# Kernel tuning notes

Hardware: AMD Instinct MI355X
Metric: run time of the kernel (lower is better)

## Reference

```python
import jax, jax.numpy as jnp
import numpy as np

N_NODES = 20000
N_EDGES = 200000
F = 132            # features_dim
DEGREES = (1, 2, 3)
REPEATS = jnp.array([3, 5, 7])   # 2l+1
EV_DIM = 15
H_INV, D_INV = 4, 33   # num_heads, inv_head_dim
H_EV, D_EV = 3, 44     # len(degrees), ev_head_dim
NRB = 32


def so3_invariants(x, y):
    # per-degree inner product over the (2l+1) components -> [E, len(degrees)]
    p = x * y
    return jnp.stack([p[:, 0:3].sum(-1), p[:, 3:8].sum(-1), p[:, 8:15].sum(-1)], axis=-1)


def filter_net(rbf, evi, Wr1, br1, Wr2, br2, We1, be1, We2, be2):
    # mlp_rbf: Linear(nrb,F)->SiLU->Linear(F,F); mlp_ev: Linear(3,F//4)->SiLU->Linear(F//4,F)
    r = jax.nn.silu(rbf @ Wr1 + br1) @ Wr2 + br2
    e = jax.nn.silu(evi @ We1 + be1) @ We2 + be2
    return r + e


def setup_inputs() -> dict:
    key = jax.random.key(0)
    ks = jax.random.split(key, 32)
    s = 0.05
    inp = {
        'inv_features': jax.random.normal(ks[0], (N_NODES, F), jnp.float32),
        'ev_features': jax.random.normal(ks[1], (N_NODES, EV_DIM), jnp.float32),
        'rbf': jax.random.uniform(ks[2], (N_EDGES, NRB), jnp.float32),
        'senders': jax.random.randint(ks[3], (N_EDGES,), 0, N_NODES, jnp.int32),
        'receivers': jax.random.randint(ks[4], (N_EDGES,), 0, N_NODES, jnp.int32),
        'sh_vectors': jax.random.normal(ks[5], (N_EDGES, EV_DIM), jnp.float32),
        'cutoffs': jax.random.uniform(ks[6], (N_EDGES, 1), jnp.float32),
        # attention weights
        'W_q_inv': jax.random.normal(ks[7], (H_INV, D_INV, D_INV), jnp.float32) * s,
        'W_k_inv': jax.random.normal(ks[8], (H_INV, D_INV, D_INV), jnp.float32) * s,
        'W_v_inv': jax.random.normal(ks[9], (H_INV, D_INV, D_INV), jnp.float32) * s,
        'W_q_ev': jax.random.normal(ks[10], (H_EV, D_EV, D_EV), jnp.float32) * s,
        'W_k_ev': jax.random.normal(ks[11], (H_EV, D_EV, D_EV), jnp.float32) * s,
    }
    # two FilterNets (inv and ev), stored as [in,out] matrices
    for tag, base in (('fi', 12), ('fe', 20)):
        inp[f'{tag}_rbf_W1'] = jax.random.normal(ks[base + 0], (NRB, F), jnp.float32) * s
        inp[f'{tag}_rbf_b1'] = jnp.zeros((F,), jnp.float32)
        inp[f'{tag}_rbf_W2'] = jax.random.normal(ks[base + 1], (F, F), jnp.float32) * s
        inp[f'{tag}_rbf_b2'] = jnp.zeros((F,), jnp.float32)
        inp[f'{tag}_ev_W1'] = jax.random.normal(ks[base + 2], (len(DEGREES), F // 4), jnp.float32) * s
        inp[f'{tag}_ev_b1'] = jnp.zeros((F // 4,), jnp.float32)
        inp[f'{tag}_ev_W2'] = jax.random.normal(ks[base + 3], (F // 4, F), jnp.float32) * s
        inp[f'{tag}_ev_b2'] = jnp.zeros((F,), jnp.float32)
    # interaction block linear: (F+len(degrees)) -> (F+len(degrees))
    inp['W_int'] = jax.random.normal(ks[28], (F + len(DEGREES), F + len(DEGREES)), jnp.float32) * s
    inp['b_int'] = jnp.zeros((F + len(DEGREES),), jnp.float32)
    return inp


def _forward(inv_features, ev_features, rbf, sh_vectors, cutoffs,
             W_q_inv, W_k_inv, W_v_inv, W_q_ev, W_k_ev,
             fi, fe, W_int, b_int, senders, receivers):
    E = rbf.shape[0]
    N = inv_features.shape[0]
    # ---- EuclideanAttentionBlock ----
    ev_diff = ev_features[senders] - ev_features[receivers]          # [E, 15]
    evi = so3_invariants(ev_diff, ev_diff)                            # [E, 3]
    fw_inv = filter_net(rbf, evi, *fi).reshape(E, H_INV, D_INV)
    fw_ev = filter_net(rbf, evi, *fe).reshape(E, H_EV, D_EV)
    x_inv = inv_features.reshape(N, H_INV, D_INV)
    x_ev = inv_features.reshape(N, H_EV, D_EV)
    q_inv = jnp.einsum('Hij,NHi->NHj', W_q_inv, x_inv)[receivers]
    k_inv = jnp.einsum('Hij,NHi->NHj', W_k_inv, x_inv)[senders]
    v_inv = jnp.einsum('Hij,NHi->NHj', W_v_inv, x_inv)[senders]
    q_ev = jnp.einsum('Hij,NHi->NHj', W_q_ev, x_ev)[receivers]
    k_ev = jnp.einsum('Hij,NHi->NHj', W_k_ev, x_ev)[senders]
    alpha_inv = (q_inv * k_inv * fw_inv).sum(-1, keepdims=True) / np.sqrt(D_INV)  # [E,H,1]
    scaled_inv = cutoffs[:, None] * alpha_inv * v_inv                 # [E,H,D]
    d_inv = jax.ops.segment_sum(scaled_inv, receivers, num_segments=N).reshape(N, F)
    alpha_ev = (q_ev * k_ev * fw_ev).sum(-1) / np.sqrt(D_EV)          # [E,3]
    alpha_ev = jnp.repeat(alpha_ev, REPEATS, axis=-1, total_repeat_length=EV_DIM)
    d_ev = jax.ops.segment_sum(cutoffs * alpha_ev * sh_vectors, receivers, num_segments=N)
    att_inv = inv_features + d_inv
    att_ev = ev_features + d_ev
    # ---- InteractionBlock ----
    evi2 = so3_invariants(att_ev, att_ev)                             # [N,3]
    t = jnp.concatenate([att_inv, evi2], axis=-1) @ W_int + b_int
    d_inv2, b_ev = t[:, :F], t[:, F:]
    d_ev2 = jnp.repeat(b_ev, REPEATS, axis=-1, total_repeat_length=EV_DIM) * att_ev
    return att_inv + d_inv2, att_ev + d_ev2


def reference(inv_features, ev_features, rbf, senders, receivers, sh_vectors, cutoffs,
              W_q_inv, W_k_inv, W_v_inv, W_q_ev, W_k_ev,
              fi_rbf_W1, fi_rbf_b1, fi_rbf_W2, fi_rbf_b2, fi_ev_W1, fi_ev_b1, fi_ev_W2, fi_ev_b2,
              fe_rbf_W1, fe_rbf_b1, fe_rbf_W2, fe_rbf_b2, fe_ev_W1, fe_ev_b1, fe_ev_W2, fe_ev_b2,
              W_int, b_int):
    fi = (fi_rbf_W1, fi_rbf_b1, fi_rbf_W2, fi_rbf_b2, fi_ev_W1, fi_ev_b1, fi_ev_W2, fi_ev_b2)
    fe = (fe_rbf_W1, fe_rbf_b1, fe_rbf_W2, fe_rbf_b2, fe_ev_W1, fe_ev_b1, fe_ev_W2, fe_ev_b2)
    return _forward(inv_features, ev_features, rbf, sh_vectors, cutoffs,
                    W_q_inv, W_k_inv, W_v_inv, W_q_ev, W_k_ev,
                    fi, fe, W_int, b_int, senders, receivers)
```

## Files before the change

kernel.cpp:

```cpp
#include <hip/hip_runtime.h>


#define NN 20000
#define NE 200000
#define FD 132
#define RB 32
#define EVD 15
#define TE 64
#define KPAD 200
#define KG 192
#define NP 144
#define PNT 28
#define FNT 28

typedef __attribute__((ext_vector_type(8))) short bf16x8;
typedef __attribute__((ext_vector_type(4))) float f32x4;

__device__ __forceinline__ float silu_f(float x) {
    return x / (1.0f + __expf(-x));
}
__device__ __forceinline__ unsigned short f2bf(float x) {
    union { float f; unsigned u; } v; v.f = x;
    unsigned r = v.u + 0x7FFF + ((v.u >> 16) & 1);
    return (unsigned short)(r >> 16);
}

__global__ __launch_bounds__(256) void k_prep(
    const float* __restrict__ Wq, const float* __restrict__ Wk, const float* __restrict__ Wv,
    const float* __restrict__ fiW1, const float* __restrict__ fiW2, const float* __restrict__ fiWe2,
    const float* __restrict__ feW1, const float* __restrict__ feW2, const float* __restrict__ feWe2,
    unsigned short* __restrict__ W1Tfi, unsigned short* __restrict__ W1Tfe,
    unsigned short* __restrict__ W2Tfi, unsigned short* __restrict__ W2Tfe,
    float* __restrict__ WqP, float* __restrict__ WkP, float* __restrict__ WvP)
{
    const int gid = blockIdx.x * 256 + threadIdx.x;
    const int gs  = gridDim.x * 256;
    for (int idx = gid; idx < NP * RB; idx += gs) {
        int n = idx / RB, k = idx - n * RB;
        W1Tfi[idx] = f2bf((n < FD) ? fiW1[k * FD + n] : 0.0f);
        W1Tfe[idx] = f2bf((n < FD) ? feW1[k * FD + n] : 0.0f);
    }
    for (int idx = gid; idx < NP * KG; idx += gs) {
        int n = idx / KG, k = idx - n * KG;
        float vi = 0.0f, ve = 0.0f;
        if (n < FD) {
            if (k < FD)       { vi = fiW2[k * FD + n];          ve = feW2[k * FD + n]; }
            else if (k < 165) { vi = fiWe2[(k - FD) * FD + n];  ve = feWe2[(k - FD) * FD + n]; }
        }
        W2Tfi[idx] = f2bf(vi);
        W2Tfe[idx] = f2bf(ve);
    }
    for (int idx = gid; idx < 4 * 33 * 36; idx += gs) {
        int H = idx / (33 * 36), rem = idx - H * (33 * 36);
        int i = rem / 36, jp = rem - i * 36;
        float q = 0.f, k = 0.f, v = 0.f;
        if (jp < 33) {
            q = Wq[H * 1089 + i * 33 + jp];
            k = Wk[H * 1089 + i * 33 + jp];
            v = Wv[H * 1089 + i * 33 + jp];
        }
        WqP[idx] = q; WkP[idx] = k; WvP[idx] = v;
    }
}

__device__ __forceinline__ void proj_inv_pass(
    const float* __restrict__ wb, const float (*__restrict__ xT)[PNT],
    float* __restrict__ outp, int t, int n0)
{
    const int q = t % 36, g = t / 36;
    if (g >= 7) return;
    const int H = q / 9, jb = (q - H * 9) * 4, nb = g * 4;
    const int fb = H * 33;
    float acc[4][4] = {};
    for (int i = 0; i < 33; ++i) {
        const float4 w = *(const float4*)&wb[(fb + i) * 36 + jb];
        const float4 x = *(const float4*)&xT[fb + i][nb];
        const float xs[4] = {x.x, x.y, x.z, x.w};
        const float ws[4] = {w.x, w.y, w.z, w.w};
        #pragma unroll
        for (int r = 0; r < 4; ++r)
            #pragma unroll
            for (int c = 0; c < 4; ++c)
                acc[r][c] = fmaf(ws[c], xs[r], acc[r][c]);
    }
    #pragma unroll
    for (int c = 0; c < 4; ++c) {
        int jj = jb + c;
        if (jj >= 33) break;
        int j = H * 33 + jj;
        #pragma unroll
        for (int r = 0; r < 4; ++r) {
            int n = n0 + nb + r;
            if (n < NN) outp[n * FD + j] = acc[r][c];
        }
    }
}

__device__ __forceinline__ void proj_ev_pass(
    const float* __restrict__ wb, const float (*__restrict__ xT)[PNT],
    float* __restrict__ outp, int t, int n0)
{
    const int q = t % 33, g = t / 33;
    if (g >= 7) return;
    const int H = q / 11, jb = (q - H * 11) * 4, nb = g * 4;
    const int fb = H * 44;
    float acc[4][4] = {};
    for (int i = 0; i < 44; ++i) {
        const float4 w = *(const float4*)&wb[(fb + i) * 44 + jb];
        const float4 x = *(const float4*)&xT[fb + i][nb];
        const float xs[4] = {x.x, x.y, x.z, x.w};
        const float ws[4] = {w.x, w.y, w.z, w.w};
        #pragma unroll
        for (int r = 0; r < 4; ++r)
            #pragma unroll
            for (int c = 0; c < 4; ++c)
                acc[r][c] = fmaf(ws[c], xs[r], acc[r][c]);
    }
    #pragma unroll
    for (int c = 0; c < 4; ++c) {
        int j = fb + jb + c;
        #pragma unroll
        for (int r = 0; r < 4; ++r) {
            int n = n0 + nb + r;
            if (n < NN) outp[n * FD + j] = acc[r][c];
        }
    }
}

__global__ __launch_bounds__(256) void k_proj(
    const float* __restrict__ xin,
    const float* __restrict__ WqP, const float* __restrict__ WkP, const float* __restrict__ WvP,
    const float* __restrict__ Wqe, const float* __restrict__ Wke,
    float* __restrict__ qinv, float* __restrict__ kinv, float* __restrict__ vinv,
    float* __restrict__ qev, float* __restrict__ kev)
{
    __shared__ __align__(16) float xT[FD][PNT];
    __shared__ __align__(16) float wb[5808];
    const int t = threadIdx.x;
    const int n0 = blockIdx.x * PNT;

    for (int idx = t; idx < PNT * FD; idx += 256) {
        int nl = idx / FD, j = idx - nl * FD;
        int n = n0 + nl;
        xT[j][nl] = (n < NN) ? xin[n * FD + j] : 0.0f;
    }
    for (int idx = t; idx < 4752; idx += 256) wb[idx] = WqP[idx];
    __syncthreads();
    proj_inv_pass(wb, xT, qinv, t, n0);
    __syncthreads();
    for (int idx = t; idx < 4752; idx += 256) wb[idx] = WkP[idx];
    __syncthreads();
    proj_inv_pass(wb, xT, kinv, t, n0);
    __syncthreads();
    for (int idx = t; idx < 4752; idx += 256) wb[idx] = WvP[idx];
    __syncthreads();
    proj_inv_pass(wb, xT, vinv, t, n0);
    __syncthreads();
    for (int idx = t; idx < 5808; idx += 256) wb[idx] = Wqe[idx];
    __syncthreads();
    proj_ev_pass(wb, xT, qev, t, n0);
    __syncthreads();
    for (int idx = t; idx < 5808; idx += 256) wb[idx] = Wke[idx];
    __syncthreads();
    proj_ev_pass(wb, xT, kev, t, n0);
}

__global__ __launch_bounds__(256) void k_evi(
    const float* __restrict__ ev, const int* __restrict__ snd,
    const int* __restrict__ rcv, float* __restrict__ evi)
{
    int e = blockIdx.x * 256 + threadIdx.x;
    if (e >= NE) return;
    int s = snd[e], r = rcv[e];
    const float* ps = &ev[s * EVD];
    const float* pr = &ev[r * EVD];
    float s0 = 0.f, s1 = 0.f, s2 = 0.f;
    #pragma unroll
    for (int m = 0; m < 3; ++m)  { float d = ps[m] - pr[m]; s0 = fmaf(d, d, s0); }
    #pragma unroll
    for (int m = 3; m < 8; ++m)  { float d = ps[m] - pr[m]; s1 = fmaf(d, d, s1); }
    #pragma unroll
    for (int m = 8; m < 15; ++m) { float d = ps[m] - pr[m]; s2 = fmaf(d, d, s2); }
    evi[e * 3 + 0] = s0; evi[e * 3 + 1] = s1; evi[e * 3 + 2] = s2;
}

template<int PATH>
__global__ __launch_bounds__(256, 4) void k_edge(
    const float* __restrict__ rbf, const float* __restrict__ evi,
    const int* __restrict__ snd, const int* __restrict__ rcv,
    const float* __restrict__ cut, const float* __restrict__ sh,
    const unsigned short* __restrict__ W1T,
    const float* __restrict__ b1,
    const unsigned short* __restrict__ W2T,
    const float* __restrict__ b2,
    const float* __restrict__ We1, const float* __restrict__ be1,
    const float* __restrict__ be2,
    const float* __restrict__ qt, const float* __restrict__ kt,
    const float* __restrict__ vt, float* __restrict__ dout)
{
    __shared__ __align__(16) char lds_buf[TE * FD * 4];
    __shared__ float evl[TE * 3];
    __shared__ int   sl[TE];
    __shared__ int   rl[TE];
    __shared__ float cl[TE];
    __shared__ float al[TE * 4];

    typedef unsigned short (*HTp)[KPAD];
    HTp HT   = (HTp)lds_buf;
    float* FW = (float*)lds_buf;

    const int t    = threadIdx.x;
    const int wv   = t >> 6;
    const int ln   = t & 63;
    const int lrow = ln & 15;
    const int kseg = ln >> 4;
    const int e0   = blockIdx.x * TE;

    if (t < TE) {
        sl[t] = snd[e0 + t];
        rl[t] = rcv[e0 + t];
        cl[t] = cut[e0 + t];
    }
    for (int idx = t; idx < TE * 3; idx += 256) evl[idx] = evi[e0 * 3 + idx];
    __syncthreads();

    {
        const int erow = e0 + 16 * wv + lrow;
        const float4 ra = *(const float4*)&rbf[erow * RB + kseg * 8];
        const float4 rb = *(const float4*)&rbf[erow * RB + kseg * 8 + 4];
        bf16x8 afrag;
        afrag[0] = (short)f2bf(ra.x); afrag[1] = (short)f2bf(ra.y);
        afrag[2] = (short)f2bf(ra.z); afrag[3] = (short)f2bf(ra.w);
        afrag[4] = (short)f2bf(rb.x); afrag[5] = (short)f2bf(rb.y);
        afrag[6] = (short)f2bf(rb.z); afrag[7] = (short)f2bf(rb.w);
        #pragma unroll
        for (int nt = 0; nt < 9; ++nt) {
            const int ncol = nt * 16 + lrow;
            bf16x8 bfrag = *(const bf16x8*)&W1T[ncol * RB + kseg * 8];
            f32x4 acc = {0.f, 0.f, 0.f, 0.f};
            acc = __builtin_amdgcn_mfma_f32_16x16x32_bf16(afrag, bfrag, acc, 0, 0, 0);
            if (ncol < FD) {
                const float bias = b1[ncol];
                #pragma unroll
                for (int r = 0; r < 4; ++r)
                    HT[16 * wv + kseg * 4 + r][ncol] = f2bf(silu_f(acc[r] + bias));
            }
        }
    }
    for (int idx = t; idx < TE * 33; idx += 256) {
        int e = idx / 33, ii = idx - e * 33;
        float a = be1[ii];
        a = fmaf(evl[e * 3 + 0], We1[ii], a);
        a = fmaf(evl[e * 3 + 1], We1[33 + ii], a);
        a = fmaf(evl[e * 3 + 2], We1[66 + ii], a);
        HT[e][FD + ii] = f2bf(silu_f(a));
    }
    for (int idx = t; idx < TE * (KPAD - 165); idx += 256) {
        int e = idx / (KPAD - 165), kk = idx - e * (KPAD - 165);
        HT[e][165 + kk] = 0;
    }
    __syncthreads();

    f32x4 acc[9];
    #pragma unroll
    for (int nt = 0; nt < 9; ++nt) acc[nt] = (f32x4){0.f, 0.f, 0.f, 0.f};
    {
        const unsigned short* hrow = &HT[16 * wv + lrow][0];
        #pragma unroll
        for (int kt = 0; kt < 6; ++kt) {
            bf16x8 afrag = *(const bf16x8*)&hrow[kt * 32 + kseg * 8];
            #pragma unroll
            for (int nt = 0; nt < 9; ++nt) {
                bf16x8 bfrag = *(const bf16x8*)&W2T[(nt * 16 + lrow) * KG + kt * 32 + kseg * 8];
                acc[nt] = __builtin_amdgcn_mfma_f32_16x16x32_bf16(afrag, bfrag, acc[nt], 0, 0, 0);
            }
        }
    }
    __syncthreads();

    #pragma unroll
    for (int nt = 0; nt < 9; ++nt) {
        const int ncol = nt * 16 + lrow;
        if (ncol < FD) {
            const float bias = b2[ncol] + be2[ncol];
            #pragma unroll
            for (int r = 0; r < 4; ++r)
                FW[(16 * wv + kseg * 4 + r) * FD + ncol] = acc[nt][r] + bias;
        }
    }
    __syncthreads();

    for (int idx = t; idx < TE * FD; idx += 256) {
        int e = idx / FD, j = idx - e * FD;
        FW[idx] *= qt[rl[e] * FD + j] * kt[sl[e] * FD + j];
    }
    __syncthreads();

    if (PATH == 0) {
        {
            int e = t >> 2, H = t & 3;
            const float* fp = &FW[e * FD + H * 33];
            float a = 0.0f;
            #pragma unroll
            for (int j = 0; j < 33; ++j) a += fp[j];
            al[t] = a * cl[e] * 0.17407765595569785f;
        }
    } else {
        if (t < TE * 3) {
            int e = t / 3, H = t - e * 3;
            const float* fp = &FW[e * FD + H * 44];
            float a = 0.0f;
            #pragma unroll
            for (int j = 0; j < 44; ++j) a += fp[j];
            al[e * 4 + H] = a * cl[e] * 0.15075567228888181f;
        }
    }
    __syncthreads();

    if (PATH == 0) {
        for (int idx = t; idx < TE * FD; idx += 256) {
            int e = idx / FD, j = idx - e * FD;
            float v = al[e * 4 + j / 33] * vt[sl[e] * FD + j];
            atomicAdd(&dout[rl[e] * FD + j], v);
        }
    } else {
        for (int idx = t; idx < TE * EVD; idx += 256) {
            int e = idx / EVD, m = idx - e * EVD;
            int hd = (m < 3) ? 0 : ((m < 8) ? 1 : 2);
            float v = al[e * 4 + hd] * sh[(e0 + e) * EVD + m];
            atomicAdd(&dout[rl[e] * EVD + m], v);
        }
    }
}

__global__ __launch_bounds__(256) void k_final(
    const float* __restrict__ xin, const float* __restrict__ evf,
    const float* __restrict__ dinv, const float* __restrict__ dev,
    const float* __restrict__ Wint, const float* __restrict__ bint,
    float* __restrict__ out)
{
    __shared__ __align__(16) float catT[136][FNT];
    __shared__ __align__(16) float wb[45 * 136];
    __shared__ float aev[FNT][16];
    __shared__ float tacc[FNT][4];
    const int t = threadIdx.x;
    const int n0 = blockIdx.x * FNT;

    for (int idx = t; idx < FNT * FD; idx += 256) {
        int nl = idx / FD, j = idx - nl * FD;
        int n = n0 + nl;
        catT[j][nl] = (n < NN) ? xin[n * FD + j] + dinv[n * FD + j] : 0.0f;
    }
    for (int idx = t; idx < FNT * EVD; idx += 256) {
        int nl = idx / EVD, m = idx - nl * EVD;
        int n = n0 + nl;
        aev[nl][m] = (n < NN) ? evf[n * EVD + m] + dev[n * EVD + m] : 0.0f;
    }
    if (t < FNT) catT[135][t] = 0.0f;
    __syncthreads();
    if (t < FNT * 3) {
        int nl = t / 3, k = t - nl * 3;
        int lo = (k == 0) ? 0 : ((k == 1) ? 3 : 8);
        int hi = (k == 0) ? 3 : ((k == 1) ? 8 : 15);
        float s = 0.f;
        for (int m = lo; m < hi; ++m) { float v = aev[nl][m]; s = fmaf(v, v, s); }
        catT[FD + k][nl] = s;
    }

    const int q = t % 34, g = t / 34;
    const int jb = q * 4, nb = g * 4;
    const bool act = (g < 7);
    float acc[4][4] = {};
    for (int ch = 0; ch < 3; ++ch) {
        __syncthreads();
        const int rbase = ch * 45;
        for (int idx = t; idx < 45 * 136; idx += 256) {
            int r = idx / 136, j = idx - r * 136;
            wb[idx] = (j < 135) ? Wint[(rbase + r) * 135 + j] : 0.0f;
        }
        __syncthreads();
        if (act) {
            for (int c = 0; c < 45; ++c) {
                const float4 w = *(const float4*)&wb[c * 136 + jb];
                const float4 x = *(const float4*)&catT[rbase + c][nb];
                const float xs[4] = {x.x, x.y, x.z, x.w};
                const float ws[4] = {w.x, w.y, w.z, w.w};
                #pragma unroll
                for (int r = 0; r < 4; ++r)
                    #pragma unroll
                    for (int cc = 0; cc < 4; ++cc)
                        acc[r][cc] = fmaf(ws[cc], xs[r], acc[r][cc]);
            }
        }
    }
    if (act) {
        #pragma unroll
        for (int c = 0; c < 4; ++c) {
            int j = jb + c;
            if (j >= 135) break;
            float bj = bint[j];
            #pragma unroll
            for (int r = 0; r < 4; ++r) {
                int n = n0 + nb + r;
                if (n >= NN) continue;
                float a = acc[r][c] + bj;
                if (j < FD) out[n * FD + j] = catT[j][nb + r] + a;
                else        tacc[nb + r][j - FD] = a;
            }
        }
    }
    __syncthreads();
    for (int idx = t; idx < FNT * EVD; idx += 256) {
        int nl = idx / EVD, m = idx - nl * EVD;
        int n = n0 + nl;
        if (n >= NN) continue;
        int hd = (m < 3) ? 0 : ((m < 8) ? 1 : 2);
        out[NN * FD + n * EVD + m] = aev[nl][m] * (1.0f + tacc[nl][hd]);
    }
}

extern "C" void kernel_launch(void* const* d_in, const int* in_sizes, int n_in,
                              void* d_out, int out_size, void* d_ws, size_t ws_size,
                              hipStream_t stream)
{
    (void)in_sizes; (void)n_in; (void)out_size; (void)ws_size;
    const float* xin  = (const float*)d_in[0];
    const float* evf  = (const float*)d_in[1];
    const float* rbf  = (const float*)d_in[2];
    const int*   snd  = (const int*)d_in[3];
    const int*   rcv  = (const int*)d_in[4];
    const float* sh   = (const float*)d_in[5];
    const float* cut  = (const float*)d_in[6];
    const float* Wint = (const float*)d_in[28];
    const float* bint = (const float*)d_in[29];

    float* ws   = (float*)d_ws;
    float* qinv = ws;
    float* kinv = qinv + NN * FD;
    float* vinv = kinv + NN * FD;
    float* qev  = vinv + NN * FD;
    float* kev  = qev  + NN * FD;
    float* evi  = kev  + NN * FD;
    float* dinv = evi  + NE * 3;
    float* dev  = dinv + NN * FD;
    float* wtail = dev + NN * EVD;

    unsigned short* W2Tfi = (unsigned short*)wtail;
    unsigned short* W2Tfe = W2Tfi + NP * KG;
    unsigned short* W1Tfi = W2Tfe + NP * KG;
    unsigned short* W1Tfe = W1Tfi + NP * RB;
    float* WqP = (float*)(W1Tfe + NP * RB);
    float* WkP = WqP + 4 * 33 * 36;
    float* WvP = WkP + 4 * 33 * 36;

    hipMemsetAsync(dinv, 0, (size_t)(NN * FD + NN * EVD) * sizeof(float), stream);

    k_prep<<<64, 256, 0, stream>>>(
        (const float*)d_in[7], (const float*)d_in[8], (const float*)d_in[9],
        (const float*)d_in[12], (const float*)d_in[14], (const float*)d_in[18],
        (const float*)d_in[20], (const float*)d_in[22], (const float*)d_in[26],
        W1Tfi, W1Tfe, W2Tfi, W2Tfe, WqP, WkP, WvP);

    k_proj<<<(NN + PNT - 1) / PNT, 256, 0, stream>>>(
        xin, WqP, WkP, WvP,
        (const float*)d_in[10], (const float*)d_in[11],
        qinv, kinv, vinv, qev, kev);
    k_evi<<<(NE + 255) / 256, 256, 0, stream>>>(evf, snd, rcv, evi);

    const int nt = NE / TE;
    k_edge<0><<<nt, 256, 0, stream>>>(rbf, evi, snd, rcv, cut, sh,
        W1Tfi, (const float*)d_in[13], W2Tfi, (const float*)d_in[15],
        (const float*)d_in[16], (const float*)d_in[17], (const float*)d_in[19],
        qinv, kinv, vinv, dinv);
    k_edge<1><<<nt, 256, 0, stream>>>(rbf, evi, snd, rcv, cut, sh,
        W1Tfe, (const float*)d_in[21], W2Tfe, (const float*)d_in[23],
        (const float*)d_in[24], (const float*)d_in[25], (const float*)d_in[27],
        qev, kev, nullptr, dev);

    k_final<<<(NN + FNT - 1) / FNT, 256, 0, stream>>>(
        xin, evf, dinv, dev, Wint, bint, (float*)d_out);
}
```

Before: 668.9 us.

## Replace edge atomic scatter with CSR gather by receiver in final kernel

Edge kernels now write only per-edge attention coefficients instead of scattering per-edge messages into node accumulators with atomics. A histogram, single-block scan and fill build a receiver-sorted CSR edge index. The final kernel then gathers messages per node from the values and sh vectors before the interaction block. This removes about 26M float atomics and the accumulator memset. It adds three small launches, including a serial single-block scan, and irregular per-node gather loops with load imbalance.

```diff
diff --git a/kernel.cpp b/kernel.cpp
--- a/kernel.cpp
+++ b/kernel.cpp
@@ -63,6 +63,51 @@
     }
 }
 
+__global__ __launch_bounds__(256) void k_hist(const int* __restrict__ rcv,
+                                              int* __restrict__ cnt)
+{
+    int e = blockIdx.x * 256 + threadIdx.x;
+    if (e < NE) atomicAdd(&cnt[rcv[e]], 1);
+}
+
+__global__ __launch_bounds__(256) void k_scan(int* __restrict__ cnt_cursor,
+                                              int* __restrict__ roff)
+{
+    __shared__ int buf[256];
+    __shared__ int carry_s;
+    const int t = threadIdx.x;
+    if (t == 0) carry_s = 0;
+    __syncthreads();
+    for (int base = 0; base < NN; base += 256) {
+        int v = (base + t < NN) ? cnt_cursor[base + t] : 0;
+        buf[t] = v;
+        __syncthreads();
+        for (int off = 1; off < 256; off <<= 1) {
+            int add = (t >= off) ? buf[t - off] : 0;
+            __syncthreads();
+            buf[t] += add;
+            __syncthreads();
+        }
+        int ex = carry_s + buf[t] - v;
+        if (base + t < NN) { roff[base + t] = ex; cnt_cursor[base + t] = ex; }
+        __syncthreads();
+        if (t == 0) carry_s += buf[255];
+        __syncthreads();
+    }
+    if (t == 0) roff[NN] = carry_s;
+}
+
+__global__ __launch_bounds__(256) void k_fill(const int* __restrict__ rcv,
+                                              int* __restrict__ cursor,
+                                              int* __restrict__ eid)
+{
+    int e = blockIdx.x * 256 + threadIdx.x;
+    if (e < NE) {
+        int p = atomicAdd(&cursor[rcv[e]], 1);
+        eid[p] = e;
+    }
+}
+
 __device__ __forceinline__ void proj_inv_pass(
     const float* __restrict__ wb, const float (*__restrict__ xT)[PNT],
     float* __restrict__ outp, int t, int n0)
@@ -188,7 +233,7 @@
 __global__ __launch_bounds__(256, 4) void k_edge(
     const float* __restrict__ rbf, const float* __restrict__ evi,
     const int* __restrict__ snd, const int* __restrict__ rcv,
-    const float* __restrict__ cut, const float* __restrict__ sh,
+    const float* __restrict__ cut,
     const unsigned short* __restrict__ W1T,
     const float* __restrict__ b1,
     const unsigned short* __restrict__ W2T,
@@ -196,14 +241,13 @@
     const float* __restrict__ We1, const float* __restrict__ be1,
     const float* __restrict__ be2,
     const float* __restrict__ qt, const float* __restrict__ kt,
-    const float* __restrict__ vt, float* __restrict__ dout)
+    float* __restrict__ aout)
 {
     __shared__ __align__(16) char lds_buf[TE * FD * 4];
     __shared__ float evl[TE * 3];
     __shared__ int   sl[TE];
     __shared__ int   rl[TE];
     __shared__ float cl[TE];
-    __shared__ float al[TE * 4];
 
     typedef unsigned short (*HTp)[KPAD];
     HTp HT   = (HTp)lds_buf;
@@ -297,14 +341,12 @@
     __syncthreads();
 
     if (PATH == 0) {
-        {
-            int e = t >> 2, H = t & 3;
-            const float* fp = &FW[e * FD + H * 33];
-            float a = 0.0f;
-            #pragma unroll
-            for (int j = 0; j < 33; ++j) a += fp[j];
-            al[t] = a * cl[e] * 0.17407765595569785f;
-        }
+        int e = t >> 2, H = t & 3;
+        const float* fp = &FW[e * FD + H * 33];
+        float a = 0.0f;
+        #pragma unroll
+        for (int j = 0; j < 33; ++j) a += fp[j];
+        aout[(e0 + e) * 4 + H] = a * cl[e] * 0.17407765595569785f;
     } else {
         if (t < TE * 3) {
             int e = t / 3, H = t - e * 3;
@@ -312,30 +354,17 @@
             float a = 0.0f;
             #pragma unroll
             for (int j = 0; j < 44; ++j) a += fp[j];
-            al[e * 4 + H] = a * cl[e] * 0.15075567228888181f;
-        }
-    }
-    __syncthreads();
-
-    if (PATH == 0) {
-        for (int idx = t; idx < TE * FD; idx += 256) {
-            int e = idx / FD, j = idx - e * FD;
-            float v = al[e * 4 + j / 33] * vt[sl[e] * FD + j];
-            atomicAdd(&dout[rl[e] * FD + j], v);
-        }
-    } else {
-        for (int idx = t; idx < TE * EVD; idx += 256) {
-            int e = idx / EVD, m = idx - e * EVD;
-            int hd = (m < 3) ? 0 : ((m < 8) ? 1 : 2);
-            float v = al[e * 4 + hd] * sh[(e0 + e) * EVD + m];
-            atomicAdd(&dout[rl[e] * EVD + m], v);
+            aout[(e0 + e) * 4 + H] = a * cl[e] * 0.15075567228888181f;
         }
     }
 }
 
 __global__ __launch_bounds__(256) void k_final(
     const float* __restrict__ xin, const float* __restrict__ evf,
-    const float* __restrict__ dinv, const float* __restrict__ dev,
+    const float* __restrict__ vt, const float* __restrict__ sh,
+    const float* __restrict__ alphaI, const float* __restrict__ alphaE,
+    const int* __restrict__ roff, const int* __restrict__ eid,
+    const int* __restrict__ snd,
     const float* __restrict__ Wint, const float* __restrict__ bint,
     float* __restrict__ out)
 {
@@ -345,16 +374,34 @@
     __shared__ float tacc[FNT][4];
     const int t = threadIdx.x;
     const int n0 = blockIdx.x * FNT;
-
-    for (int idx = t; idx < FNT * FD; idx += 256) {
-        int nl = idx / FD, j = idx - nl * FD;
-        int n = n0 + nl;
-        catT[j][nl] = (n < NN) ? xin[n * FD + j] + dinv[n * FD + j] : 0.0f;
-    }
-    for (int idx = t; idx < FNT * EVD; idx += 256) {
-        int nl = idx / EVD, m = idx - nl * EVD;
-        int n = n0 + nl;
-        aev[nl][m] = (n < NN) ? evf[n * EVD + m] + dev[n * EVD + m] : 0.0f;
+    const int wv = t >> 6, ln = t & 63;
+
+    const int h0 = ln / 33;
+    const int h1 = (64 + ln) / 33;
+    const int hm = (ln < 3) ? 0 : ((ln < 8) ? 1 : 2);
+    for (int nl = wv; nl < FNT; nl += 4) {
+        const int n = n0 + nl;
+        float a0 = 0.f, a1 = 0.f, a2 = 0.f, dv = 0.f;
+        if (n < NN) {
+            const int pend = roff[n + 1];
+            for (int p = roff[n]; p < pend; ++p) {
+                const int e = eid[p];
+                const int s = snd[e];
+                const float* vrow = vt + s * FD;
+                a0 = fmaf(alphaI[e * 4 + h0], vrow[ln], a0);
+                a1 = fmaf(alphaI[e * 4 + h1], vrow[64 + ln], a1);
+                if (ln < 4)  a2 = fmaf(alphaI[e * 4 + 3], vrow[128 + ln], a2);
+                if (ln < 15) dv = fmaf(alphaE[e * 4 + hm], sh[e * EVD + ln], dv);
+            }
+            catT[ln][nl]      = xin[n * FD + ln]      + a0;
+            catT[64 + ln][nl] = xin[n * FD + 64 + ln] + a1;
+            if (ln < 4)  catT[128 + ln][nl] = xin[n * FD + 128 + ln] + a2;
+            if (ln < 15) aev[nl][ln] = evf[n * EVD + ln] + dv;
+        } else {
+            catT[ln][nl] = 0.f; catT[64 + ln][nl] = 0.f;
+            if (ln < 4)  catT[128 + ln][nl] = 0.f;
+            if (ln < 15) aev[nl][ln] = 0.f;
+        }
     }
     if (t < FNT) catT[135][t] = 0.0f;
     __syncthreads();
@@ -434,16 +481,20 @@
     const float* Wint = (const float*)d_in[28];
     const float* bint = (const float*)d_in[29];
 
-    float* ws   = (float*)d_ws;
-    float* qinv = ws;
-    float* kinv = qinv + NN * FD;
-    float* vinv = kinv + NN * FD;
-    float* qev  = vinv + NN * FD;
-    float* kev  = qev  + NN * FD;
-    float* evi  = kev  + NN * FD;
-    float* dinv = evi  + NE * 3;
-    float* dev  = dinv + NN * FD;
-    float* wtail = dev + NN * EVD;
+    float* ws     = (float*)d_ws;
+    float* qinv   = ws;
+    float* kinv   = qinv   + NN * FD;
+    float* vinv   = kinv   + NN * FD;
+    float* qev    = vinv   + NN * FD;
+    float* kev    = qev    + NN * FD;
+    float* evi    = kev    + NN * FD;
+    float* alphaI = evi    + NE * 3;
+    float* alphaE = alphaI + NE * 4;
+    int*   iwork  = (int*)(alphaE + NE * 4);
+    int*   roff   = iwork;
+    int*   cnt_cursor = roff + (NN + 1);
+    int*   eid    = cnt_cursor + NN;
+    float* wtail  = (float*)(iwork + 240004);
 
     unsigned short* W2Tfi = (unsigned short*)wtail;
     unsigned short* W2Tfe = W2Tfi + NP * KG;
@@ -453,7 +504,10 @@
     float* WkP = WqP + 4 * 33 * 36;
     float* WvP = WkP + 4 * 33 * 36;
 
-    hipMemsetAsync(dinv, 0, (size_t)(NN * FD + NN * EVD) * sizeof(float), stream);
+    hipMemsetAsync(cnt_cursor, 0, (size_t)NN * sizeof(int), stream);
+    k_hist<<<(NE + 255) / 256, 256, 0, stream>>>(rcv, cnt_cursor);
+    k_scan<<<1, 256, 0, stream>>>(cnt_cursor, roff);
+    k_fill<<<(NE + 255) / 256, 256, 0, stream>>>(rcv, cnt_cursor, eid);
 
     k_prep<<<64, 256, 0, stream>>>(
         (const float*)d_in[7], (const float*)d_in[8], (const float*)d_in[9],
@@ -468,15 +522,16 @@
     k_evi<<<(NE + 255) / 256, 256, 0, stream>>>(evf, snd, rcv, evi);
 
     const int nt = NE / TE;
-    k_edge<0><<<nt, 256, 0, stream>>>(rbf, evi, snd, rcv, cut, sh,
+    k_edge<0><<<nt, 256, 0, stream>>>(rbf, evi, snd, rcv, cut,
         W1Tfi, (const float*)d_in[13], W2Tfi, (const float*)d_in[15],
         (const float*)d_in[16], (const float*)d_in[17], (const float*)d_in[19],
-        qinv, kinv, vinv, dinv);
-    k_edge<1><<<nt, 256, 0, stream>>>(rbf, evi, snd, rcv, cut, sh,
+        qinv, kinv, alphaI);
+    k_edge<1><<<nt, 256, 0, stream>>>(rbf, evi, snd, rcv, cut,
         W1Tfe, (const float*)d_in[21], W2Tfe, (const float*)d_in[23],
         (const float*)d_in[24], (const float*)d_in[25], (const float*)d_in[27],
-        qev, kev, nullptr, dev);
+        qev, kev, alphaE);
 
     k_final<<<(NN + FNT - 1) / FNT, 256, 0, stream>>>(
-        xin, evf, dinv, dev, Wint, bint, (float*)d_out);
-}
+        xin, evf, vinv, sh, alphaI, alphaE, roff, eid, snd,
+        Wint, bint, (float*)d_out);
+}
```

Result: slower. 763.9 us (+14.2%).
